# Kernel optimization log

Hardware: AMD Instinct MI355X
Metric: run time of the kernel (lower is better)

Reference implementation:

```python
import jax, jax.numpy as jnp
import numpy as np

D_MODEL = 1024
NUM_HEADS = 16
HEAD_DIM = D_MODEL // NUM_HEADS


def setup_inputs() -> dict:
    key = jax.random.key(0)
    k1, k2, k3, k4, k5 = jax.random.split(key, 5)
    scale = 1.0 / np.sqrt(D_MODEL)
    x = jax.random.normal(k1, (8, 1024, D_MODEL), dtype=jnp.float32)
    # weights stored (in, out) so y = x @ W + b (same math as torch Linear)
    Wqkv = jax.random.normal(k2, (D_MODEL, 3 * D_MODEL), dtype=jnp.float32) * scale
    bqkv = jax.random.normal(k3, (3 * D_MODEL,), dtype=jnp.float32) * scale
    Wo = jax.random.normal(k4, (D_MODEL, D_MODEL), dtype=jnp.float32) * scale
    bo = jax.random.normal(k5, (D_MODEL,), dtype=jnp.float32) * scale
    return {"x": x, "Wqkv": Wqkv, "bqkv": bqkv, "Wo": Wo, "bo": bo}


def reference(x, Wqkv, bqkv, Wo, bo):
    B, S, D = x.shape
    H, Hd = NUM_HEADS, HEAD_DIM
    # fused QKV projection: [B,S,3D]
    qkv = jnp.einsum('bsd,de->bse', x, Wqkv) + bqkv
    # reshape -> [B,S,H,3*Hd] -> [B,H,S,3*Hd], then chunk
    qkv = qkv.reshape(B, S, H, 3 * Hd).transpose(0, 2, 1, 3)
    q, k, v = jnp.split(qkv, 3, axis=-1)  # each [B,H,S,Hd]
    scores = jnp.einsum('bhqd,bhkd->bhqk', q, k) / jnp.sqrt(jnp.asarray(Hd, x.dtype))
    attn = jax.nn.softmax(scores, axis=-1)
    vals = jnp.einsum('bhqk,bhkd->bhqd', attn, v)  # [B,H,S,Hd]
    vals = vals.transpose(0, 2, 1, 3).reshape(B, S, D)
    out = jnp.einsum('bsd,de->bse', vals, Wo) + bo
    return out
```

## Files before the change

kernel.cpp:

```cpp
#include <hip/hip_runtime.h>
#include <hip/hip_bf16.h>
#include <stdint.h>


typedef __bf16 bf16;
typedef __bf16 bf16x4 __attribute__((ext_vector_type(4)));
typedef __bf16 bf16x8 __attribute__((ext_vector_type(8)));
typedef float f32x4 __attribute__((ext_vector_type(4)));

__device__ __forceinline__ void async_copy16(const bf16* g, bf16* l) {
  void* gv = (void*)g;
  __builtin_amdgcn_global_load_lds((__attribute__((address_space(1))) void*)gv,
                                   (__attribute__((address_space(3))) void*)l,
                                   16, 0, 0);
}

__device__ __forceinline__ void wt_body(const float* __restrict__ in,
                                        bf16* __restrict__ out,
                                        int R, int C, int bx, int by,
                                        int tid, bf16 (*tile)[65]) {
  const int c0 = bx * 64, r0 = by * 64;
  const int c = tid & 63, g = tid >> 6;
#pragma unroll
  for (int j = 0; j < 16; j++) {
    int r = j * 4 + g;
    tile[r][c] = (bf16)in[(size_t)(r0 + r) * C + c0 + c];
  }
  __syncthreads();
#pragma unroll
  for (int j = 0; j < 16; j++) {
    int r = j * 4 + g;
    out[(size_t)(c0 + r) * R + r0 + c] = tile[c][r];
  }
}

__global__ __launch_bounds__(256) void prep_kernel(const float* __restrict__ x,
                                                   bf16* __restrict__ xb,
                                                   const float* __restrict__ Wqkv,
                                                   bf16* __restrict__ Wqkt,
                                                   const float* __restrict__ Wo,
                                                   bf16* __restrict__ Wot) {
  __shared__ bf16 tile[64][65];
  const int bid = blockIdx.x;
  const int tid = threadIdx.x;
  if (bid < 4096) {
    int i = (bid * 256 + tid) * 8;
    float4 a = *(const float4*)(x + i);
    float4 b = *(const float4*)(x + i + 4);
    bf16x8 v;
    v[0] = (bf16)a.x; v[1] = (bf16)a.y; v[2] = (bf16)a.z; v[3] = (bf16)a.w;
    v[4] = (bf16)b.x; v[5] = (bf16)b.y; v[6] = (bf16)b.z; v[7] = (bf16)b.w;
    *(bf16x8*)(xb + i) = v;
  } else if (bid < 4096 + 768) {
    int idx = bid - 4096;
    wt_body(Wqkv, Wqkt, 1024, 3072, idx % 48, idx / 48, tid, tile);
  } else {
    int idx = bid - 4864;
    wt_body(Wo, Wot, 1024, 1024, idx % 16, idx / 16, tid, tile);
  }
}

#define LS_STRIDE 136
template <typename OutT, bool WITH_VT>
__global__ __launch_bounds__(256, 2)
void gemm_bt_bias(const bf16* __restrict__ A, const bf16* __restrict__ Bt,
                  const float* __restrict__ bias, OutT* __restrict__ C,
                  bf16* __restrict__ Vt, int N, int K) {
  __shared__ __align__(16) bf16 smem[128 * 64 * 2];
  bf16* const As = smem;
  bf16* const Bs = smem + 128 * 64;
  const int tid = threadIdx.x;
  const int lane = tid & 63;
  const int w = tid >> 6;
  const int m0 = blockIdx.y * 128;
  const int n0 = blockIdx.x * 128;
  const int wm = (w & 1) * 64;
  const int wn = (w >> 1) * 64;
  const int l15 = lane & 15, g8 = lane >> 4, l7 = lane & 7;

  f32x4 acc[4][4] = {};

  const int sr = tid >> 3;
  const int scs = ((tid & 7) ^ (sr & 7)) * 8;
  const bf16* Ag = A + (size_t)(m0 + sr) * K + scs;
  const bf16* Bg = Bt + (size_t)(n0 + sr) * K + scs;

  for (int k0 = 0; k0 < K; k0 += 64) {
    __syncthreads();
#pragma unroll
    for (int m = 0; m < 4; m++) {
      async_copy16(Ag + (size_t)(32 * m) * K + k0, &As[m * 2048 + tid * 8]);
      async_copy16(Bg + (size_t)(32 * m) * K + k0, &Bs[m * 2048 + tid * 8]);
    }
    __syncthreads();
#pragma unroll
    for (int ks = 0; ks < 2; ks++) {
      const int ch = ((ks * 4 + g8) ^ l7) * 8;
      bf16x8 af[4], bfr[4];
#pragma unroll
      for (int mt = 0; mt < 4; mt++)
        af[mt] = *(const bf16x8*)&As[(wm + mt * 16 + l15) * 64 + ch];
#pragma unroll
      for (int nt = 0; nt < 4; nt++)
        bfr[nt] = *(const bf16x8*)&Bs[(wn + nt * 16 + l15) * 64 + ch];
#pragma unroll
      for (int mt = 0; mt < 4; mt++)
#pragma unroll
        for (int nt = 0; nt < 4; nt++)
          acc[mt][nt] = __builtin_amdgcn_mfma_f32_16x16x32_bf16(af[mt], bfr[nt], acc[mt][nt], 0, 0, 0);
    }
  }

  const int rowg = g8 * 4;
  int vo = -1, vh = 0;
  if (WITH_VT) {
    const int rem = n0 % 192;
    if (rem == 128) vo = 0;
    else if (rem == 64) vo = 64;
    vh = (n0 + (vo > 0 ? vo : 0)) / 192;
  }
  const bool myV = WITH_VT && (vo == wn);

#pragma unroll
  for (int nt = 0; nt < 4; nt++) {
    const int n = n0 + wn + nt * 16 + l15;
    const float bv = bias[n];
    if (!myV) {
#pragma unroll
      for (int mt = 0; mt < 4; mt++) {
        const int mbase = m0 + wm + mt * 16 + rowg;
#pragma unroll
        for (int r = 0; r < 4; r++)
          C[(size_t)(mbase + r) * N + n] = (OutT)(acc[mt][nt][r] + bv);
      }
    }
  }

  if (WITH_VT && vo >= 0) {
    __syncthreads();
    bf16* const Ls = smem;
    if (myV) {
#pragma unroll
      for (int nt = 0; nt < 4; nt++) {
        const int d = nt * 16 + l15;
        const float bv = bias[n0 + vo + d];
#pragma unroll
        for (int mt = 0; mt < 4; mt++) {
          const int sl = wm + mt * 16 + rowg;
          bf16x4 v;
#pragma unroll
          for (int r = 0; r < 4; r++) v[r] = (bf16)(acc[mt][nt][r] + bv);
          *(bf16x4*)&Ls[d * LS_STRIDE + sl] = v;
        }
      }
    }
    __syncthreads();
    const int bb = m0 >> 10, s0 = m0 & 1023;
    const int sd = tid >> 4, s8 = (tid & 15) * 8;
#pragma unroll
    for (int it = 0; it < 4; it++) {
      const int d = it * 16 + sd;
      bf16x8 v = *(const bf16x8*)&Ls[d * LS_STRIDE + s8];
      *(bf16x8*)&Vt[(((size_t)(bb * 16 + vh) * 64 + d) << 10) + s0 + s8] = v;
    }
  }
}

#define PS_STRIDE 72
__global__ __launch_bounds__(256, 4)
void attn_kernel(const bf16* __restrict__ qkv, const bf16* __restrict__ Vt,
                 bf16* __restrict__ vals) {
  __shared__ __align__(16) bf16 smem[64 * 64 * 2 + 128 * PS_STRIDE];
  bf16* const Qs = smem;
  bf16* const Ks = smem;
  bf16* const Vs = smem + 4096;
  bf16* const Ps = smem + 8192;
  const int tid = threadIdx.x;
  const int lane = tid & 63;
  const int w = tid >> 6;
  const int bh = blockIdx.x;
  const int q0 = blockIdx.y * 128;
  const int b = bh >> 4, h = bh & 15;
  const size_t tok0 = (size_t)b * 1024;
  const int l15 = lane & 15, g8 = lane >> 4, l7 = lane & 7;

  {
    const int r = tid >> 3;
    const int cs = ((tid & 7) ^ (r & 7)) * 8;
    const bf16* g = qkv + (tok0 + q0 + r) * 3072 + h * 192 + cs;
    async_copy16(g, &Qs[tid * 8]);
    async_copy16(g + (size_t)32 * 3072, &Qs[2048 + tid * 8]);
    async_copy16(g + (size_t)64 * 3072, &Qs[4096 + tid * 8]);
    async_copy16(g + (size_t)96 * 3072, &Qs[6144 + tid * 8]);
  }
  __syncthreads();

  bf16x8 aq[2][2];
#pragma unroll
  for (int ks = 0; ks < 2; ks++) {
    const int ch = ((ks * 4 + g8) ^ l7) * 8;
#pragma unroll
    for (int mt = 0; mt < 2; mt++)
      aq[mt][ks] = *(const bf16x8*)&Qs[(w * 32 + mt * 16 + l15) * 64 + ch];
  }
  __builtin_amdgcn_s_waitcnt(0xC07F);

  f32x4 O[2][4] = {};
  f32x4 lacc[2] = {};
  bf16x8 ones;
#pragma unroll
  for (int j = 0; j < 8; j++) ones[j] = (bf16)1.0f;

  const int kr = tid >> 3;
  const int kcs = ((tid & 7) ^ (kr & 7)) * 8;
  const float scale = 0.125f;

  for (int kt = 0; kt < 16; kt++) {
    const int k0 = kt * 64;
    __syncthreads();
    {
      const bf16* kg = qkv + (tok0 + k0 + kr) * 3072 + h * 192 + 64 + kcs;
      async_copy16(kg, &Ks[tid * 8]);
      async_copy16(kg + (size_t)32 * 3072, &Ks[2048 + tid * 8]);
      const bf16* vg = Vt + ((size_t)bh * 64 + kr) * 1024 + k0 + kcs;
      async_copy16(vg, &Vs[tid * 8]);
      async_copy16(vg + (size_t)32 * 1024, &Vs[2048 + tid * 8]);
    }
    __syncthreads();

    f32x4 S[2][4] = {};
#pragma unroll
    for (int ks = 0; ks < 2; ks++) {
      const int ch = ((ks * 4 + g8) ^ l7) * 8;
      bf16x8 bfr[4];
#pragma unroll
      for (int nt = 0; nt < 4; nt++)
        bfr[nt] = *(const bf16x8*)&Ks[(nt * 16 + l15) * 64 + ch];
#pragma unroll
      for (int mt = 0; mt < 2; mt++)
#pragma unroll
        for (int nt = 0; nt < 4; nt++)
          S[mt][nt] = __builtin_amdgcn_mfma_f32_16x16x32_bf16(aq[mt][ks], bfr[nt], S[mt][nt], 0, 0, 0);
    }

#pragma unroll
    for (int mt = 0; mt < 2; mt++) {
#pragma unroll
      for (int nt = 0; nt < 4; nt++) {
        int q = w * 32 + mt * 16 + g8 * 4;
        int c = nt * 16 + l15;
#pragma unroll
        for (int r = 0; r < 4; r++)
          Ps[(q + r) * PS_STRIDE + c] = (bf16)__expf(S[mt][nt][r] * scale);
      }
    }

#pragma unroll
    for (int ks = 0; ks < 2; ks++) {
      const int ch = ((ks * 4 + g8) ^ l7) * 8;
      bf16x8 af[2], bfr[4];
#pragma unroll
      for (int mt = 0; mt < 2; mt++)
        af[mt] = *(const bf16x8*)&Ps[(w * 32 + mt * 16 + l15) * PS_STRIDE + ks * 32 + g8 * 8];
#pragma unroll
      for (int dt = 0; dt < 4; dt++)
        bfr[dt] = *(const bf16x8*)&Vs[(dt * 16 + l15) * 64 + ch];
#pragma unroll
      for (int mt = 0; mt < 2; mt++) {
#pragma unroll
        for (int dt = 0; dt < 4; dt++)
          O[mt][dt] = __builtin_amdgcn_mfma_f32_16x16x32_bf16(af[mt], bfr[dt], O[mt][dt], 0, 0, 0);
        lacc[mt] = __builtin_amdgcn_mfma_f32_16x16x32_bf16(af[mt], ones, lacc[mt], 0, 0, 0);
      }
    }
  }

#pragma unroll
  for (int mt = 0; mt < 2; mt++) {
    int qb = q0 + w * 32 + mt * 16 + g8 * 4;
    f32x4 rinv;
#pragma unroll
    for (int r = 0; r < 4; r++) rinv[r] = 1.0f / lacc[mt][r];
#pragma unroll
    for (int dt = 0; dt < 4; dt++) {
      int d = h * 64 + dt * 16 + l15;
#pragma unroll
      for (int r = 0; r < 4; r++)
        vals[(tok0 + qb + r) * 1024 + d] = (bf16)(O[mt][dt][r] * rinv[r]);
    }
  }
}

extern "C" void kernel_launch(void* const* d_in, const int* in_sizes, int n_in,
                              void* d_out, int out_size, void* d_ws, size_t ws_size,
                              hipStream_t stream) {
  const float* x    = (const float*)d_in[0];
  const float* Wqkv = (const float*)d_in[1];
  const float* bqkv = (const float*)d_in[2];
  const float* Wo   = (const float*)d_in[3];
  const float* bo   = (const float*)d_in[4];
  float* out = (float*)d_out;

  uint8_t* ws = (uint8_t*)d_ws;
  bf16* qkv  = (bf16*)(ws);
  bf16* Wqkt = (bf16*)(ws + 48u * 1024 * 1024);
  bf16* Wot  = (bf16*)(ws + 54u * 1024 * 1024);
  bf16* Vt   = (bf16*)(ws + 56u * 1024 * 1024);
  bf16* vals = (bf16*)(ws + 72u * 1024 * 1024);
  bf16* xb   = (bf16*)(ws + 88u * 1024 * 1024);

  prep_kernel<<<5120, 256, 0, stream>>>(x, xb, Wqkv, Wqkt, Wo, Wot);
  gemm_bt_bias<bf16, true><<<dim3(24, 64), 256, 0, stream>>>(xb, Wqkt, bqkv, qkv, Vt, 3072, 1024);
  attn_kernel<<<dim3(128, 8), 256, 0, stream>>>(qkv, Vt, vals);
  gemm_bt_bias<float, false><<<dim3(8, 64), 256, 0, stream>>>(vals, Wot, bo, out, nullptr, 1024, 1024);
}
```

Measured before the change: 237.6 us.

## Double-buffer K/V tiles in attention and fold softmax scale into Q projection

The attention kernel now keeps two K/V shared-memory buffers and issues the async loads for the next key tile before computing on the current one, so global loads overlap with the MFMA work. This also removes one barrier per iteration. The 1/sqrt(head_dim) factor is moved into the Q columns of the transposed QKV weight and the Q bias, which removes the per-element multiply before exp. The larger LDS footprint lowers the occupancy hint from 4 to 3 blocks per CU, and that may offset the gain from overlapping loads with compute.

```diff
diff --git a/kernel.cpp b/kernel.cpp
--- a/kernel.cpp
+++ b/kernel.cpp
@@ -18,7 +18,7 @@
 __device__ __forceinline__ void wt_body(const float* __restrict__ in,
                                         bf16* __restrict__ out,
                                         int R, int C, int bx, int by,
-                                        int tid, bf16 (*tile)[65]) {
+                                        int tid, bf16 (*tile)[65], bool scale_q) {
   const int c0 = bx * 64, r0 = by * 64;
   const int c = tid & 63, g = tid >> 6;
 #pragma unroll
@@ -27,10 +27,11 @@
     tile[r][c] = (bf16)in[(size_t)(r0 + r) * C + c0 + c];
   }
   __syncthreads();
+  const float sc = scale_q ? 0.125f : 1.0f;
 #pragma unroll
   for (int j = 0; j < 16; j++) {
     int r = j * 4 + g;
-    out[(size_t)(c0 + r) * R + r0 + c] = tile[c][r];
+    out[(size_t)(c0 + r) * R + r0 + c] = (bf16)((float)tile[c][r] * sc);
   }
 }
 
@@ -53,10 +54,11 @@
     *(bf16x8*)(xb + i) = v;
   } else if (bid < 4096 + 768) {
     int idx = bid - 4096;
-    wt_body(Wqkv, Wqkt, 1024, 3072, idx % 48, idx / 48, tid, tile);
+    int bx = idx % 48;
+    wt_body(Wqkv, Wqkt, 1024, 3072, bx, idx / 48, tid, tile, (bx % 3) == 0);
   } else {
     int idx = bid - 4864;
-    wt_body(Wo, Wot, 1024, 1024, idx % 16, idx / 16, tid, tile);
+    wt_body(Wo, Wot, 1024, 1024, idx % 16, idx / 16, tid, tile, false);
   }
 }
 
@@ -124,7 +126,8 @@
 #pragma unroll
   for (int nt = 0; nt < 4; nt++) {
     const int n = n0 + wn + nt * 16 + l15;
-    const float bv = bias[n];
+    float bv = bias[n];
+    if (WITH_VT && (((n >> 6) % 3) == 0)) bv *= 0.125f;
     if (!myV) {
 #pragma unroll
       for (int mt = 0; mt < 4; mt++) {
@@ -167,14 +170,12 @@
 }
 
 #define PS_STRIDE 72
-__global__ __launch_bounds__(256, 4)
+__global__ __launch_bounds__(256, 3)
 void attn_kernel(const bf16* __restrict__ qkv, const bf16* __restrict__ Vt,
                  bf16* __restrict__ vals) {
-  __shared__ __align__(16) bf16 smem[64 * 64 * 2 + 128 * PS_STRIDE];
+  __shared__ __align__(16) bf16 smem[8192 * 2 + 128 * PS_STRIDE];
   bf16* const Qs = smem;
-  bf16* const Ks = smem;
-  bf16* const Vs = smem + 4096;
-  bf16* const Ps = smem + 8192;
+  bf16* const Ps = smem + 16384;
   const int tid = threadIdx.x;
   const int lane = tid & 63;
   const int w = tid >> 6;
@@ -183,6 +184,8 @@
   const int b = bh >> 4, h = bh & 15;
   const size_t tok0 = (size_t)b * 1024;
   const int l15 = lane & 15, g8 = lane >> 4, l7 = lane & 7;
+  const int kr = tid >> 3;
+  const int kcs = ((tid & 7) ^ (kr & 7)) * 8;
 
   {
     const int r = tid >> 3;
@@ -204,6 +207,7 @@
       aq[mt][ks] = *(const bf16x8*)&Qs[(w * 32 + mt * 16 + l15) * 64 + ch];
   }
   __builtin_amdgcn_s_waitcnt(0xC07F);
+  __syncthreads();
 
   f32x4 O[2][4] = {};
   f32x4 lacc[2] = {};
@@ -211,22 +215,25 @@
 #pragma unroll
   for (int j = 0; j < 8; j++) ones[j] = (bf16)1.0f;
 
-  const int kr = tid >> 3;
-  const int kcs = ((tid & 7) ^ (kr & 7)) * 8;
-  const float scale = 0.125f;
+  auto stageKV = [&](int kt) {
+    bf16* Kb = smem + (kt & 1) * 8192;
+    bf16* Vb = Kb + 4096;
+    const int k0 = kt * 64;
+    const bf16* kg = qkv + (tok0 + k0 + kr) * 3072 + h * 192 + 64 + kcs;
+    async_copy16(kg, &Kb[tid * 8]);
+    async_copy16(kg + (size_t)32 * 3072, &Kb[2048 + tid * 8]);
+    const bf16* vg = Vt + ((size_t)bh * 64 + kr) * 1024 + k0 + kcs;
+    async_copy16(vg, &Vb[tid * 8]);
+    async_copy16(vg + (size_t)32 * 1024, &Vb[2048 + tid * 8]);
+  };
+
+  stageKV(0);
 
   for (int kt = 0; kt < 16; kt++) {
-    const int k0 = kt * 64;
-    __syncthreads();
-    {
-      const bf16* kg = qkv + (tok0 + k0 + kr) * 3072 + h * 192 + 64 + kcs;
-      async_copy16(kg, &Ks[tid * 8]);
-      async_copy16(kg + (size_t)32 * 3072, &Ks[2048 + tid * 8]);
-      const bf16* vg = Vt + ((size_t)bh * 64 + kr) * 1024 + k0 + kcs;
-      async_copy16(vg, &Vs[tid * 8]);
-      async_copy16(vg + (size_t)32 * 1024, &Vs[2048 + tid * 8]);
-    }
-    __syncthreads();
+    __syncthreads();
+    if (kt < 15) stageKV(kt + 1);
+    bf16* const Ks = smem + (kt & 1) * 8192;
+    bf16* const Vs = Ks + 4096;
 
     f32x4 S[2][4] = {};
 #pragma unroll
@@ -251,7 +258,7 @@
         int c = nt * 16 + l15;
 #pragma unroll
         for (int r = 0; r < 4; r++)
-          Ps[(q + r) * PS_STRIDE + c] = (bf16)__expf(S[mt][nt][r] * scale);
+          Ps[(q + r) * PS_STRIDE + c] = (bf16)__expf(S[mt][nt][r]);
       }
     }
 
```

Result: faster. 227.9 us (-4.1%).
